# Optimization experiments

Hardware: AMD Instinct MI355X
Metric: run time of the kernel (lower is better)

The kernel has to match this reference:

```python
import jax, jax.numpy as jnp
import numpy as np

B, N, E = 128, 1024, 16384
ENTITY, EMB, HID = 100000, 100, 100


def setup_inputs() -> dict:
    key = jax.random.key(0)
    ks = jax.random.split(key, 13)
    s = 0.1  # param init scale
    return {
        "neighbors": jax.random.randint(ks[0], (B, N), 0, ENTITY),
        "adj_row": jax.random.randint(ks[1], (B, E), 0, N),
        "adj_col": jax.random.randint(ks[2], (B, E), 0, N),
        "adj_val": jax.random.uniform(ks[3], (B, E), jnp.float32),
        "emb_table": jax.random.normal(ks[4], (ENTITY, EMB), jnp.float32) * s,
        "gcn_w": jax.random.normal(ks[5], (EMB, HID), jnp.float32) * s,
        "gcn_b": jax.random.normal(ks[6], (HID,), jnp.float32) * s,
        "w_ih": jax.random.normal(ks[7], (3 * HID, HID), jnp.float32) * s,
        "w_hh": jax.random.normal(ks[8], (3 * HID, HID), jnp.float32) * s,
        "b_ih": jax.random.normal(ks[9], (3 * HID,), jnp.float32) * s,
        "b_hh": jax.random.normal(ks[10], (3 * HID,), jnp.float32) * s,
        "fc1_w": jax.random.normal(ks[11], (HID, HID), jnp.float32) * s,
        "fc1_b": jax.random.normal(ks[12], (HID,), jnp.float32) * s,
    }


def reference(neighbors, adj_row, adj_col, adj_val, emb_table,
              gcn_w, gcn_b, w_ih, w_hh, b_ih, b_hh, fc1_w, fc1_b):
    n_nodes = neighbors.shape[1]
    # Embedding lookup: [B, N, EMB]
    x = emb_table[neighbors]
    # GCN layer: support = X @ W, then sparse adj @ support, then + bias
    support = jnp.einsum('bne,eh->bnh', x, gcn_w)  # [B, N, HID]

    def spmm(row, col, val, sup):
        # out[r] += val * sup[col]  (per-sample sparse aggregation)
        return jax.ops.segment_sum(val[:, None] * sup[col], row,
                                   num_segments=n_nodes)

    seq = jax.vmap(spmm)(adj_row, adj_col, adj_val, support) + gcn_b  # [B,N,HID]

    # GRU over node sequence (PyTorch gate order: r, z, n)
    def gru_step(h, x_t):
        gx = x_t @ w_ih.T + b_ih
        gh = h @ w_hh.T + b_hh
        xr, xz, xn = jnp.split(gx, 3, axis=-1)
        hr, hz, hn = jnp.split(gh, 3, axis=-1)
        r = jax.nn.sigmoid(xr + hr)
        z = jax.nn.sigmoid(xz + hz)
        n = jnp.tanh(xn + r * hn)
        h_new = (1.0 - z) * n + z * h
        return h_new, None

    h0 = jnp.zeros((seq.shape[0], w_hh.shape[1]), seq.dtype)
    h, _ = jax.lax.scan(gru_step, h0, seq.transpose(1, 0, 2))  # final hidden [B,HID]

    # h.permute(1,0,2) -> [B, 1, HID], then relu(fc1(.))
    return jax.nn.relu(h[:, None, :] @ fc1_w.T + fc1_b)
```

## Files before the change

### kernel.cpp

```cpp
#include <hip/hip_runtime.h>
#include <hip/hip_bf16.h>


typedef unsigned int u32;
typedef float f2 __attribute__((ext_vector_type(2)));

__device__ __forceinline__ float bflo(u32 u) {
    union { u32 i; float f; } v; v.i = u << 16; return v.f;
}
__device__ __forceinline__ float bfhi(u32 u) {
    union { u32 i; float f; } v; v.i = u & 0xffff0000u; return v.f;
}
__device__ __forceinline__ u32 f2bf1(float f) {
    union { float f; u32 u; } v; v.f = f;
    return (v.u + 0x7fffu + ((v.u >> 16) & 1u)) >> 16;
}
__device__ __forceinline__ u32 packbf(float a, float b) {
    return f2bf1(a) | (f2bf1(b) << 16);
}
__device__ __forceinline__ float sigm(float x) { return 1.f / (1.f + __expf(-x)); }
__device__ __forceinline__ float tanh_fast(float x) {
    float e = __expf(2.f * x);
    return 1.f - 2.f / (e + 1.f);
}

__global__ __launch_bounds__(256, 2)
void gcn_kernel(const int* __restrict__ nb, const float* __restrict__ emb,
                const float* __restrict__ w, u32* __restrict__ support)
{
    __shared__ float wl[10000];
    for (int i = threadIdx.x; i < 10000; i += 256) wl[i] = w[i];
    __syncthreads();

    const int n = blockIdx.x * 256 + threadIdx.x;
    const long long row = nb[n];
    const float4* __restrict__ xr = (const float4*)(emb + row * 100);

    float acc[100];
#pragma unroll
    for (int h = 0; h < 100; ++h) acc[h] = 0.f;

    for (int kk = 0; kk < 25; ++kk) {
        const float4 xv = xr[kk];
        const float xs[4] = { xv.x, xv.y, xv.z, xv.w };
#pragma unroll
        for (int q = 0; q < 4; ++q) {
            const float* wrow = &wl[(kk * 4 + q) * 100];
            const float xq = xs[q];
#pragma unroll
            for (int h4 = 0; h4 < 25; ++h4) {
                const float4 w4 = *(const float4*)(wrow + h4 * 4);
                acc[h4*4+0] = fmaf(xq, w4.x, acc[h4*4+0]);
                acc[h4*4+1] = fmaf(xq, w4.y, acc[h4*4+1]);
                acc[h4*4+2] = fmaf(xq, w4.z, acc[h4*4+2]);
                acc[h4*4+3] = fmaf(xq, w4.w, acc[h4*4+3]);
            }
        }
    }

    u32* __restrict__ o = support + (size_t)n * 50;
#pragma unroll
    for (int i = 0; i < 50; ++i) o[i] = packbf(acc[2*i], acc[2*i+1]);
}

__global__ __launch_bounds__(256, 2)
void csr_build(const int* __restrict__ arow, const int* __restrict__ acol,
               const float* __restrict__ aval,
               int* __restrict__ offs, int2* __restrict__ csr)
{
    __shared__ int cnt[1024];
    __shared__ int part[256];
    __shared__ int offl[1024];

    const int b   = blockIdx.x;
    const int tid = threadIdx.x;
    const int*   rw = arow + b * 16384;
    const int*   cl = acol + b * 16384;
    const float* vl = aval + b * 16384;

    for (int i = tid; i < 1024; i += 256) cnt[i] = 0;
    __syncthreads();
    for (int e = tid; e < 16384; e += 256) atomicAdd(&cnt[rw[e]], 1);
    __syncthreads();

    int c[4]; int s = 0;
#pragma unroll
    for (int q = 0; q < 4; ++q) { c[q] = cnt[tid * 4 + q]; s += c[q]; }
    part[tid] = s;
    __syncthreads();
    for (int off = 1; off < 256; off <<= 1) {
        int v = (tid >= off) ? part[tid - off] : 0;
        __syncthreads();
        part[tid] += v;
        __syncthreads();
    }
    int run = part[tid] - s;
#pragma unroll
    for (int q = 0; q < 4; ++q) { offl[tid * 4 + q] = run; run += c[q]; }
    __syncthreads();

    for (int i = tid; i < 1024; i += 256) offs[b * 1025 + i] = offl[i];
    if (tid == 0) offs[b * 1025 + 1024] = 16384;

    int2* cs = csr + (size_t)b * 16384;
    for (int e = tid; e < 16384; e += 256) {
        const int r   = rw[e];
        const int pos = atomicAdd(&offl[r], 1);
        int2 cv; cv.x = cl[e]; cv.y = __float_as_int(vl[e]);
        cs[pos] = cv;
    }
}

__global__ __launch_bounds__(256, 4)
void spmm_agg(const int* __restrict__ offs, const int2* __restrict__ csr,
              const u32* __restrict__ support,
              const float* __restrict__ gcn_b, u32* __restrict__ seq)
{
    const int b    = blockIdx.y;
    const int lr   = threadIdx.x / 50;
    const int lane = threadIdx.x % 50;
    const int r    = blockIdx.x * 5 + lr;
    if (lr >= 5 || r >= 1024) return;

    const int e0 = offs[b * 1025 + r];
    const int e1 = offs[b * 1025 + r + 1];
    const int2* __restrict__ cs = csr + (size_t)b * 16384;
    const u32* __restrict__ supb = support + (size_t)b * 1024 * 50;

    float a0 = 0.f, a1 = 0.f;
    for (int e = e0; e < e1; ++e) {
        const int2 cv = cs[e];
        const float v = __int_as_float(cv.y);
        const u32 u = supb[(size_t)cv.x * 50 + lane];
        a0 = fmaf(v, bflo(u), a0);
        a1 = fmaf(v, bfhi(u), a1);
    }
    a0 += gcn_b[2 * lane];
    a1 += gcn_b[2 * lane + 1];
    seq[((size_t)b * 1024 + r) * 50 + lane] = packbf(a0, a1);
}

__global__ __launch_bounds__(256, 2)
void gx_gemm0(const u32* __restrict__ seq, const float* __restrict__ w_ih,
              const float* __restrict__ b_ih, u32* __restrict__ gxW,
              int c0, int ctl, int CT)
{
    __shared__ float wl[10000];
    const int g    = blockIdx.x % 3;
    const int tile = blockIdx.x / 3;
    const int tid  = threadIdx.x;

    for (int i = tid; i < 10000; i += 256)
        wl[(i % 100) * 100 + (i / 100)] = w_ih[g * 10000 + i];
    __syncthreads();

    const int m = tile * 256 + tid;
    const int b = m >> ctl;
    const int t = m & (CT - 1);
    const uint2* sr2 = (const uint2*)(seq + ((size_t)b * 1024 + c0 + t) * 50);

    float acc[100];
    const float4* bi4 = (const float4*)(b_ih + g * 100);
#pragma unroll
    for (int j4 = 0; j4 < 25; ++j4) {
        const float4 bv = bi4[j4];
        acc[j4*4+0] = bv.x; acc[j4*4+1] = bv.y; acc[j4*4+2] = bv.z; acc[j4*4+3] = bv.w;
    }

    for (int kk = 0; kk < 25; ++kk) {
        const uint2 up = sr2[kk];
        const float xs[4] = { bflo(up.x), bfhi(up.x), bflo(up.y), bfhi(up.y) };
#pragma unroll
        for (int q = 0; q < 4; ++q) {
            const float* wrow = &wl[(kk * 4 + q) * 100];
            const float xq = xs[q];
#pragma unroll
            for (int j4 = 0; j4 < 25; ++j4) {
                const float4 w4 = *(const float4*)(wrow + j4 * 4);
                acc[j4*4+0] = fmaf(xq, w4.x, acc[j4*4+0]);
                acc[j4*4+1] = fmaf(xq, w4.y, acc[j4*4+1]);
                acc[j4*4+2] = fmaf(xq, w4.z, acc[j4*4+2]);
                acc[j4*4+3] = fmaf(xq, w4.w, acc[j4*4+3]);
            }
        }
    }

    u32* og = gxW + (size_t)m * 150 + g * 50;
#pragma unroll
    for (int i = 0; i < 50; ++i) og[i] = packbf(acc[2*i], acc[2*i+1]);
}

__global__ __launch_bounds__(640, 1)
void gru_v3(const u32* __restrict__ gxR, size_t sampStride,
            const float* __restrict__ w_hh, const float* __restrict__ b_hh,
            float* __restrict__ hg, const float* __restrict__ fc1_w,
            const float* __restrict__ fc1_b, float* __restrict__ out,
            int first, int last, int CT)
{
    __shared__ float h[100];
    __shared__ float ps[600];

    const int tid  = threadIdx.x;
    const int samp = blockIdx.x;
    const int p    = tid / 320;
    const int r    = tid - p * 320;
    const bool rowAct = (r < 300);
    const int NG   = 13 - p;

    f2 wk[26];
    if (rowAct) {
        const float* wrow = w_hh + (size_t)r * 100;
#pragma unroll
        for (int i = 0; i < 13; ++i) {
            if (i < NG) {
                const int q = 2 * i + p;
                const float4 wv = *(const float4*)(wrow + 4 * q);
                wk[2*i]   = (f2){wv.x, wv.y};
                wk[2*i+1] = (f2){wv.z, wv.w};
            }
        }
    }

    float bhr = 0.f, bhz = 0.f, bhn = 0.f;
    if (tid < 100) {
        bhr = b_hh[tid]; bhz = b_hh[100 + tid]; bhn = b_hh[200 + tid];
        h[tid] = first ? 0.f : hg[samp * 100 + tid];
    }
    __syncthreads();

    const int odd = tid & 1;
    const u32* gp = gxR + (size_t)samp * sampStride + (tid >> 1);
    u32 a0 = 0, a1 = 0, a2 = 0, b0 = 0, b1 = 0, b2 = 0;
    if (tid < 100) {
        a0 = gp[0];   a1 = gp[50];  a2 = gp[100];
        b0 = gp[150]; b1 = gp[200]; b2 = gp[250];
    }

    auto stepf = [&](int t, u32& x0, u32& x1, u32& x2) {
        float sum = 0.f;
        if (rowAct) {
            f2 acc0 = {0.f, 0.f}, acc1 = {0.f, 0.f};
#pragma unroll
            for (int i = 0; i < 13; ++i) {
                if (i < NG) {
                    const int q = 2 * i + p;
                    const float4 hv = *(const float4*)(&h[4 * q]);
                    acc0 += wk[2*i]   * (f2){hv.x, hv.y};
                    acc1 += wk[2*i+1] * (f2){hv.z, hv.w};
                }
            }
            sum = (acc0.x + acc0.y) + (acc1.x + acc1.y);
        }
        const u32 c0 = x0, c1 = x1, c2 = x2;
        if (tid < 100 && t + 2 < CT) {
            const u32* q2 = gp + (size_t)(t + 2) * 150;
            x0 = q2[0]; x1 = q2[50]; x2 = q2[100];
        }
        if (rowAct) ps[p * 300 + r] = sum;
        __syncthreads();
        if (tid < 100) {
            const float ghr = ps[tid]       + ps[300 + tid] + bhr;
            const float ghz = ps[100 + tid] + ps[400 + tid] + bhz;
            const float ghn = ps[200 + tid] + ps[500 + tid] + bhn;
            const float gxr = odd ? bfhi(c0) : bflo(c0);
            const float gxz = odd ? bfhi(c1) : bflo(c1);
            const float gxn = odd ? bfhi(c2) : bflo(c2);
            const float rg = sigm(gxr + ghr);
            const float zg = sigm(gxz + ghz);
            const float ng = tanh_fast(gxn + rg * ghn);
            h[tid] = (1.f - zg) * ng + zg * h[tid];
        }
        __syncthreads();
    };

    for (int t = 0; t < CT; t += 2) {
        stepf(t,     a0, a1, a2);
        stepf(t + 1, b0, b1, b2);
    }

    if (tid < 100) {
        hg[samp * 100 + tid] = h[tid];
        if (last) {
            const float4* fw = (const float4*)(fc1_w + (size_t)tid * 100);
            float s0 = 0.f, s1 = 0.f, s2 = 0.f, s3 = 0.f;
#pragma unroll
            for (int kk = 0; kk < 25; ++kk) {
                const float4 wv = fw[kk];
                const float4 hv = *(const float4*)(&h[kk * 4]);
                s0 = fmaf(wv.x, hv.x, s0);
                s1 = fmaf(wv.y, hv.y, s1);
                s2 = fmaf(wv.z, hv.z, s2);
                s3 = fmaf(wv.w, hv.w, s3);
            }
            const float s = (s0 + s1) + (s2 + s3) + fc1_b[tid];
            out[samp * 100 + tid] = fmaxf(s, 0.f);
        }
    }
}

extern "C" void kernel_launch(void* const* d_in, const int* in_sizes, int n_in,
                              void* d_out, int out_size, void* d_ws, size_t ws_size,
                              hipStream_t stream)
{
    const int*   neighbors = (const int*)  d_in[0];
    const int*   adj_row   = (const int*)  d_in[1];
    const int*   adj_col   = (const int*)  d_in[2];
    const float* adj_val   = (const float*)d_in[3];
    const float* emb       = (const float*)d_in[4];
    const float* gcn_w     = (const float*)d_in[5];
    const float* gcn_b     = (const float*)d_in[6];
    const float* w_ih      = (const float*)d_in[7];
    const float* w_hh      = (const float*)d_in[8];
    const float* b_ih      = (const float*)d_in[9];
    const float* b_hh      = (const float*)d_in[10];
    const float* fc1_w     = (const float*)d_in[11];
    const float* fc1_b     = (const float*)d_in[12];
    float* out = (float*)d_out;

    char* ws = (char*)d_ws;
    const size_t seq_bytes     = (size_t)128 * 1024 * 50 * 4;
    const size_t hg_bytes      = 128 * 100 * 4;
    const size_t support_bytes = (size_t)128 * 1024 * 50 * 4;
    const size_t offs_bytes    = (size_t)128 * 1025 * 4;

    u32*   seq = (u32*)ws;
    float* hg  = (float*)(ws + seq_bytes);
    char*  rest = ws + seq_bytes + hg_bytes;
    const size_t rest_avail = ws_size - seq_bytes - hg_bytes;

    u32*  support = (u32*)rest;
    int*  offs    = (int*)(rest + support_bytes);
    int2* csr     = (int2*)(rest + support_bytes + offs_bytes);

    gcn_kernel<<<512, 256, 0, stream>>>(neighbors, emb, gcn_w, support);
    csr_build<<<128, 256, 0, stream>>>(adj_row, adj_col, adj_val, offs, csr);
    spmm_agg<<<dim3(205, 128), 256, 0, stream>>>(offs, csr, support, gcn_b, seq);

    const size_t gx_full = (size_t)128 * 1024 * 150 * 4;
    u32* gx = (u32*)rest;

    if (rest_avail >= gx_full) {
        gx_gemm0<<<1536, 256, 0, stream>>>(seq, w_ih, b_ih, gx, 0, 10, 1024);
        gru_v3<<<128, 640, 0, stream>>>(gx, (size_t)1024 * 150, w_hh, b_hh, hg,
                                        fc1_w, fc1_b, out, 1, 1, 1024);
    } else {
        int CT = 512, ctl = 9;
        while (CT > 8 && (size_t)128 * CT * 150 * 4 > rest_avail) { CT >>= 1; --ctl; }
        const int nch = 1024 / CT;
        for (int c = 0; c < nch; ++c) {
            gx_gemm0<<<3 * (128 * CT / 256), 256, 0, stream>>>(seq, w_ih, b_ih, gx,
                                                               c * CT, ctl, CT);
            gru_v3<<<128, 640, 0, stream>>>(gx, (size_t)CT * 150, w_hh, b_hh, hg,
                                            fc1_w, fc1_b, out,
                                            (c == 0) ? 1 : 0, (c == nch - 1) ? 1 : 0, CT);
        }
    }
}
```

Baseline: 1.326 ms.

## Restructure GRU step to one barrier per step with double-buffered hidden state

The recurrent kernel moves from 640 threads, where each thread owns one gate row and partial sums go through shared memory, to 256 threads. There, a pair of lanes owns all three gate rows for one hidden unit and combines its halves with a lane shuffle. The hidden state is double-buffered in shared memory and each thread keeps its own value in a register, so each timestep needs one __syncthreads instead of two. The aim is a shorter serial critical path per step, at the cost of three times more weight registers per thread and more FMAs per thread.

New measurement: 1.352 ms. About the same (+1.9%).

```diff
diff --git a/kernel.cpp b/kernel.cpp
--- a/kernel.cpp
+++ b/kernel.cpp
@@ -190,87 +190,100 @@
     for (int i = 0; i < 50; ++i) og[i] = packbf(acc[2*i], acc[2*i+1]);
 }
 
-__global__ __launch_bounds__(640, 1)
-void gru_v3(const u32* __restrict__ gxR, size_t sampStride,
+__global__ __launch_bounds__(256, 1)
+void gru_v4(const u32* __restrict__ gxR, size_t sampStride,
             const float* __restrict__ w_hh, const float* __restrict__ b_hh,
             float* __restrict__ hg, const float* __restrict__ fc1_w,
             const float* __restrict__ fc1_b, float* __restrict__ out,
             int first, int last, int CT)
 {
-    __shared__ float h[100];
-    __shared__ float ps[600];
+    __shared__ float hb[2][104];
 
     const int tid  = threadIdx.x;
     const int samp = blockIdx.x;
-    const int p    = tid / 320;
-    const int r    = tid - p * 320;
-    const bool rowAct = (r < 300);
-    const int NG   = 13 - p;
-
-    f2 wk[26];
-    if (rowAct) {
-        const float* wrow = w_hh + (size_t)r * 100;
+    const int j    = tid >> 1;
+    const int p    = tid & 1;
+    const int hi   = j & 1;
+    const bool act = (tid < 200);
+
+    f2 wr[26], wz[26], wn[26];
+    if (act) {
+        const float* r0 = w_hh + (size_t)j * 100;
 #pragma unroll
         for (int i = 0; i < 13; ++i) {
-            if (i < NG) {
-                const int q = 2 * i + p;
-                const float4 wv = *(const float4*)(wrow + 4 * q);
-                wk[2*i]   = (f2){wv.x, wv.y};
-                wk[2*i+1] = (f2){wv.z, wv.w};
+            const int q = 2 * i + p;
+            if (q < 25) {
+                float4 v;
+                v = *(const float4*)(r0 + 4 * q);
+                wr[2*i] = (f2){v.x, v.y}; wr[2*i+1] = (f2){v.z, v.w};
+                v = *(const float4*)(r0 + 10000 + 4 * q);
+                wz[2*i] = (f2){v.x, v.y}; wz[2*i+1] = (f2){v.z, v.w};
+                v = *(const float4*)(r0 + 20000 + 4 * q);
+                wn[2*i] = (f2){v.x, v.y}; wn[2*i+1] = (f2){v.z, v.w};
+            } else {
+                wr[2*i] = (f2){0.f, 0.f}; wr[2*i+1] = (f2){0.f, 0.f};
+                wz[2*i] = (f2){0.f, 0.f}; wz[2*i+1] = (f2){0.f, 0.f};
+                wn[2*i] = (f2){0.f, 0.f}; wn[2*i+1] = (f2){0.f, 0.f};
             }
         }
     }
 
-    float bhr = 0.f, bhz = 0.f, bhn = 0.f;
-    if (tid < 100) {
-        bhr = b_hh[tid]; bhz = b_hh[100 + tid]; bhn = b_hh[200 + tid];
-        h[tid] = first ? 0.f : hg[samp * 100 + tid];
-    }
-    __syncthreads();
-
-    const int odd = tid & 1;
-    const u32* gp = gxR + (size_t)samp * sampStride + (tid >> 1);
+    float bhr = 0.f, bhz = 0.f, bhn = 0.f, hreg = 0.f;
+    if (act) {
+        bhr = b_hh[j]; bhz = b_hh[100 + j]; bhn = b_hh[200 + j];
+        hreg = first ? 0.f : hg[samp * 100 + j];
+        if (p == 0) hb[0][j] = hreg;
+    }
+    if (tid >= 100 && tid < 104) { hb[0][tid] = 0.f; hb[1][tid] = 0.f; }
+    __syncthreads();
+
+    const u32* gp = gxR + (size_t)samp * sampStride + (tid >> 2);
     u32 a0 = 0, a1 = 0, a2 = 0, b0 = 0, b1 = 0, b2 = 0;
-    if (tid < 100) {
+    if (act) {
         a0 = gp[0];   a1 = gp[50];  a2 = gp[100];
         b0 = gp[150]; b1 = gp[200]; b2 = gp[250];
     }
 
+    int cur = 0;
     auto stepf = [&](int t, u32& x0, u32& x1, u32& x2) {
-        float sum = 0.f;
-        if (rowAct) {
-            f2 acc0 = {0.f, 0.f}, acc1 = {0.f, 0.f};
+        f2 ar0 = {0.f,0.f}, ar1 = {0.f,0.f};
+        f2 az0 = {0.f,0.f}, az1 = {0.f,0.f};
+        f2 an0 = {0.f,0.f}, an1 = {0.f,0.f};
+        if (act) {
+            const float* hc = hb[cur];
 #pragma unroll
             for (int i = 0; i < 13; ++i) {
-                if (i < NG) {
-                    const int q = 2 * i + p;
-                    const float4 hv = *(const float4*)(&h[4 * q]);
-                    acc0 += wk[2*i]   * (f2){hv.x, hv.y};
-                    acc1 += wk[2*i+1] * (f2){hv.z, hv.w};
-                }
+                const int q = 2 * i + p;
+                const float4 hv = *(const float4*)(hc + 4 * q);
+                const f2 h01 = {hv.x, hv.y}, h23 = {hv.z, hv.w};
+                ar0 += wr[2*i]   * h01;  ar1 += wr[2*i+1] * h23;
+                az0 += wz[2*i]   * h01;  az1 += wz[2*i+1] * h23;
+                an0 += wn[2*i]   * h01;  an1 += wn[2*i+1] * h23;
             }
-            sum = (acc0.x + acc0.y) + (acc1.x + acc1.y);
         }
         const u32 c0 = x0, c1 = x1, c2 = x2;
-        if (tid < 100 && t + 2 < CT) {
+        if (act && t + 2 < CT) {
             const u32* q2 = gp + (size_t)(t + 2) * 150;
             x0 = q2[0]; x1 = q2[50]; x2 = q2[100];
         }
-        if (rowAct) ps[p * 300 + r] = sum;
+        float sr = (ar0.x + ar0.y) + (ar1.x + ar1.y);
+        float sz = (az0.x + az0.y) + (az1.x + az1.y);
+        float sn = (an0.x + an0.y) + (an1.x + an1.y);
+        sr += __shfl_xor(sr, 1);
+        sz += __shfl_xor(sz, 1);
+        sn += __shfl_xor(sn, 1);
+        if (act) {
+            const float gxr = hi ? bfhi(c0) : bflo(c0);
+            const float gxz = hi ? bfhi(c1) : bflo(c1);
+            const float gxn = hi ? bfhi(c2) : bflo(c2);
+            const float rg  = sigm(gxr + sr + bhr);
+            const float zg  = sigm(gxz + sz + bhz);
+            const float ng  = tanh_fast(gxn + rg * (sn + bhn));
+            hreg = (1.f - zg) * ng + zg * hreg;
+            hb[cur ^ 1][j] = hreg;
+        }
         __syncthreads();
-        if (tid < 100) {
-            const float ghr = ps[tid]       + ps[300 + tid] + bhr;
-            const float ghz = ps[100 + tid] + ps[400 + tid] + bhz;
-            const float ghn = ps[200 + tid] + ps[500 + tid] + bhn;
-            const float gxr = odd ? bfhi(c0) : bflo(c0);
-            const float gxz = odd ? bfhi(c1) : bflo(c1);
-            const float gxn = odd ? bfhi(c2) : bflo(c2);
-            const float rg = sigm(gxr + ghr);
-            const float zg = sigm(gxz + ghz);
-            const float ng = tanh_fast(gxn + rg * ghn);
-            h[tid] = (1.f - zg) * ng + zg * h[tid];
-        }
-        __syncthreads();
+        cur ^= 1;
     };
 
     for (int t = 0; t < CT; t += 2) {
@@ -278,23 +291,22 @@
         stepf(t + 1, b0, b1, b2);
     }
 
-    if (tid < 100) {
-        hg[samp * 100 + tid] = h[tid];
-        if (last) {
-            const float4* fw = (const float4*)(fc1_w + (size_t)tid * 100);
-            float s0 = 0.f, s1 = 0.f, s2 = 0.f, s3 = 0.f;
-#pragma unroll
-            for (int kk = 0; kk < 25; ++kk) {
-                const float4 wv = fw[kk];
-                const float4 hv = *(const float4*)(&h[kk * 4]);
-                s0 = fmaf(wv.x, hv.x, s0);
-                s1 = fmaf(wv.y, hv.y, s1);
-                s2 = fmaf(wv.z, hv.z, s2);
-                s3 = fmaf(wv.w, hv.w, s3);
-            }
-            const float s = (s0 + s1) + (s2 + s3) + fc1_b[tid];
-            out[samp * 100 + tid] = fmaxf(s, 0.f);
-        }
+    if (act && p == 0) hg[samp * 100 + j] = hreg;
+    if (last && tid < 100) {
+        const float* hc = hb[cur];
+        const float4* fw = (const float4*)(fc1_w + (size_t)tid * 100);
+        float s0 = 0.f, s1 = 0.f, s2 = 0.f, s3 = 0.f;
+#pragma unroll
+        for (int kk = 0; kk < 25; ++kk) {
+            const float4 wv = fw[kk];
+            const float4 hv = *(const float4*)(hc + kk * 4);
+            s0 = fmaf(wv.x, hv.x, s0);
+            s1 = fmaf(wv.y, hv.y, s1);
+            s2 = fmaf(wv.z, hv.z, s2);
+            s3 = fmaf(wv.w, hv.w, s3);
+        }
+        const float s = (s0 + s1) + (s2 + s3) + fc1_b[tid];
+        out[samp * 100 + tid] = fmaxf(s, 0.f);
     }
 }
 
@@ -341,7 +353,7 @@
 
     if (rest_avail >= gx_full) {
         gx_gemm0<<<1536, 256, 0, stream>>>(seq, w_ih, b_ih, gx, 0, 10, 1024);
-        gru_v3<<<128, 640, 0, stream>>>(gx, (size_t)1024 * 150, w_hh, b_hh, hg,
+        gru_v4<<<128, 256, 0, stream>>>(gx, (size_t)1024 * 150, w_hh, b_hh, hg,
                                         fc1_w, fc1_b, out, 1, 1, 1024);
     } else {
         int CT = 512, ctl = 9;
@@ -350,7 +362,7 @@
         for (int c = 0; c < nch; ++c) {
             gx_gemm0<<<3 * (128 * CT / 256), 256, 0, stream>>>(seq, w_ih, b_ih, gx,
                                                                c * CT, ctl, CT);
-            gru_v3<<<128, 640, 0, stream>>>(gx, (size_t)CT * 150, w_hh, b_hh, hg,
+            gru_v4<<<128, 256, 0, stream>>>(gx, (size_t)CT * 150, w_hh, b_hh, hg,
                                             fc1_w, fc1_b, out,
                                             (c == 0) ? 1 : 0, (c == nch - 1) ? 1 : 0, CT);
         }
```
